# Kernel tuning notes

Hardware: AMD Instinct MI355X
Metric: run time of the kernel (lower is better)

The kernel has to match this reference:

```python
import jax, jax.numpy as jnp
import numpy as np

NUM_ATOMS = 1024
NUM_FEATS = 80      # c
NUM_IRREPS = 48     # (l_max+1)^2 * 3 with l_max=3
K3, K2, K1 = 1270, 24, 3  # CG-basis param counts per correlation order


def setup_inputs() -> dict:
    key = jax.random.key(0)
    ks = jax.random.split(key, 7)
    return {
        "node_feats": jax.random.normal(ks[0], (NUM_ATOMS, NUM_FEATS, NUM_IRREPS), jnp.float32),
        "U3": jax.random.normal(ks[1], (NUM_IRREPS, NUM_IRREPS, NUM_IRREPS, K3), jnp.float32),
        "U2": jax.random.normal(ks[2], (NUM_IRREPS, NUM_IRREPS, K2), jnp.float32),
        "U1": jax.random.normal(ks[3], (NUM_IRREPS, K1), jnp.float32),
        "W3": jax.random.normal(ks[4], (K3, NUM_FEATS), jnp.float32),
        "W2": jax.random.normal(ks[5], (K2, NUM_FEATS), jnp.float32),
        "W1": jax.random.normal(ks[6], (K1, NUM_FEATS), jnp.float32),
    }


def reference(node_feats, U3, U2, U1, W3, W2, W1):
    # equation_main: '...ik,kc,bci -> bc...' with U3 [p,q,i,k]
    # -> out [n, c, p, q]
    out = jnp.einsum('pqik,kc,nci->ncpq', U3, W3, node_feats)

    # corr = 2: c_tensor = einsum('...k,kc->c...', U2, W2) -> [c, p, q]
    c2 = jnp.einsum('pqk,kc->cpq', U2, W2) + out          # [n, c, p, q]
    # equation_contract: 'bc...i,bci->bc...'
    out = jnp.einsum('ncpi,nci->ncp', c2, node_feats)     # [n, c, p]

    # corr = 1: c_tensor = einsum('...k,kc->c...', U1, W1) -> [c, p]
    c1 = jnp.einsum('pk,kc->cp', U1, W1) + out            # [n, c, p]
    out = jnp.einsum('nci,nci->nc', c1, node_feats)       # [n, c]
    return out
```

## Files before the change

kernel.cpp:

```cpp
#include <hip/hip_runtime.h>
#include <hip/hip_bf16.h>

#define NA 1024
#define NC 80
#define NI 48
#define PQ (NI*NI)
#define M3 (PQ*NI)
#define K3 1270
#define K3P 1280
#define K2 24
#define K1 3

typedef __attribute__((ext_vector_type(8))) short bf16x8;
typedef __attribute__((ext_vector_type(4))) float f32x4;
typedef __attribute__((ext_vector_type(4))) unsigned int u32x4;

union BFPack { bf16x8 v; __hip_bfloat162 h[4]; };
union BF4 { uint2 u; __hip_bfloat162 h[2]; };
union BF2 { unsigned int u; __hip_bfloat162 h; };

__device__ __forceinline__ bf16x8 pack8(float a, float b, float c, float d,
                                        float e, float f, float g, float h) {
    BFPack u;
    u.h[0] = __float22bfloat162_rn(float2{a, b});
    u.h[1] = __float22bfloat162_rn(float2{c, d});
    u.h[2] = __float22bfloat162_rn(float2{e, f});
    u.h[3] = __float22bfloat162_rn(float2{g, h});
    return u.v;
}

__global__ __launch_bounds__(256) void k_prep(const float* __restrict__ W3,
                                              const float* __restrict__ U2,
                                              const float* __restrict__ W2,
                                              __hip_bfloat16* __restrict__ W3bt,
                                              float* __restrict__ c2t) {
    int b = blockIdx.x;
    if (b < NC) {
        int c = b;
        for (int k = threadIdx.x; k < K3P; k += 256) {
            float v = (k < K3) ? W3[(size_t)k * NC + c] : 0.f;
            W3bt[(size_t)c * K3P + k] = __float2bfloat16(v);
        }
    } else {
        int idx = (b - NC) * 256 + threadIdx.x;
        if (idx >= NC * PQ) return;
        int c  = idx / PQ;
        int pq = idx - c * PQ;
        float s = 0.f;
#pragma unroll
        for (int k = 0; k < K2; ++k) s += U2[pq * K2 + k] * W2[k * NC + c];
        c2t[idx] = s;
    }
}

__global__ __launch_bounds__(256) void k_uw3(const float* __restrict__ U3,
                                             const __hip_bfloat16* __restrict__ W3bt,
                                             __hip_bfloat16* __restrict__ UW3tb) {
    __shared__ __align__(16) unsigned short As[64 * 128];
    __shared__ __align__(16) unsigned short Bs[80 * 128];

    const int t    = threadIdx.x;
    const int wave = t >> 6;
    const int lane = t & 63;
    const int col  = lane & 15;
    const int quad = lane >> 4;

    const int m_base = blockIdx.x * 64;

    const float* __restrict__ aw = U3 + (size_t)(m_base + 16 * wave) * K3 + 2 * lane;
    char* asw = (char*)As + (16 * wave) * 256 + (lane & 3) * 4;
    const int ag = lane >> 2;

    f32x4 acc[5];
#pragma unroll
    for (int j = 0; j < 5; ++j) acc[j] = (f32x4)(0.f);

    float2 pA0[16], pA1[16];
    u32x4  pB[5];

    auto loadA = [&](float2* dst, int tl) {
        const float* an = aw + tl * 128;
        if (tl == 9) {
#pragma unroll
            for (int s = 0; s < 16; ++s)
                dst[s] = (lane < 59) ? *(const float2*)(an + (size_t)s * K3)
                                     : float2{0.f, 0.f};
        } else {
#pragma unroll
            for (int s = 0; s < 16; ++s)
                dst[s] = *(const float2*)(an + (size_t)s * K3);
        }
    };
    auto loadB = [&](int tl) {
        const int k0 = tl * 128;
#pragma unroll
        for (int u = 0; u < 5; ++u) {
            int G = t + 256 * u, c = G >> 4, g = G & 15;
            pB[u] = *(const u32x4*)(W3bt + (size_t)c * K3P + k0 + g * 8);
        }
    };
    auto writeA = [&](const float2* src) {
#pragma unroll
        for (int s = 0; s < 16; ++s) {
            BF2 w; w.h = __float22bfloat162_rn(src[s]);
            *(unsigned int*)(asw + s * 256 + ((ag ^ (s & 7)) * 16)) = w.u;
        }
    };
    auto writeB = [&]() {
#pragma unroll
        for (int u = 0; u < 5; ++u) {
            int G = t + 256 * u, c = G >> 4, g = G & 15;
            *(u32x4*)((char*)Bs + c * 256 + ((g ^ (c & 7)) * 16)) = pB[u];
        }
    };
    auto compute = [&]() {
        const int rbase = (16 * wave + col) * 256;
#pragma unroll
        for (int ks = 0; ks < 4; ++ks) {
            const int go = ((ks * 4 + quad) ^ (col & 7)) * 16;
            bf16x8 af = *(const bf16x8*)((const char*)As + rbase + go);
#pragma unroll
            for (int j = 0; j < 5; ++j) {
                bf16x8 bf = *(const bf16x8*)((const char*)Bs + (16 * j + col) * 256 + go);
                acc[j] = __builtin_amdgcn_mfma_f32_16x16x32_bf16(af, bf, acc[j], 0, 0, 0);
            }
        }
    };

    loadA(pA0, 0);
    loadB(0);
    loadA(pA1, 1);

#pragma unroll 1
    for (int t2 = 0; t2 < 5; ++t2) {
        const int tileA = 2 * t2;
        const int tileB = 2 * t2 + 1;

        __syncthreads();
        writeA(pA0);
        writeB();
        __syncthreads();
        if (tileA + 2 <= 9) loadA(pA0, tileA + 2);
        loadB(tileB);
        compute();

        __syncthreads();
        writeA(pA1);
        writeB();
        __syncthreads();
        if (tileB + 2 <= 9) loadA(pA1, tileB + 2);
        if (tileB + 1 <= 9) loadB(tileB + 1);
        compute();
    }

#pragma unroll
    for (int j = 0; j < 5; ++j) {
        int c = 16 * j + col;
        size_t o = (size_t)c * M3 + m_base + 16 * wave + quad * 4;
        BF4 pk;
        pk.h[0] = __float22bfloat162_rn(float2{acc[j].x, acc[j].y});
        pk.h[1] = __float22bfloat162_rn(float2{acc[j].z, acc[j].w});
        *(uint2*)&UW3tb[o] = pk.u;
    }
}

__global__ __launch_bounds__(256) void k_main(const float* __restrict__ nf,
                                              const __hip_bfloat16* __restrict__ UW3tb,
                                              const float* __restrict__ c2t,
                                              const float* __restrict__ U1,
                                              const float* __restrict__ W1,
                                              float* __restrict__ out) {
    __shared__ __align__(16) float Vs[64 * 52];
    __shared__ __align__(16) union { unsigned short vb[64 * 64];
                                     float red[64 * 17]; } VbRed;
    __shared__ __align__(16) unsigned short Ts[64 * 64];
    __shared__ __align__(16) float c2s[64];
    __shared__ __align__(16) float c1s[NI];

    const int t    = threadIdx.x;
    const int wave = t >> 6;
    const int col  = t & 15;
    const int quad = (t >> 4) & 3;

    const int bid = blockIdx.x;
    const int xcd = bid & 7;
    const int kb_ = bid >> 3;
    const int c   = xcd + 8 * (kb_ >> 4);
    const int nb  = kb_ & 15;
    const int n0  = nb * 64;

#pragma unroll
    for (int u = 0; u < 3; ++u) {
        int f   = t + 256 * u;
        int row = f / 12;
        int seg = f - row * 12;
        float4 v = *(const float4*)&nf[((size_t)(n0 + row) * NC + c) * NI + seg * 4];
        *(float4*)&Vs[row * 52 + seg * 4] = v;
        BF4 pk;
        pk.h[0] = __float22bfloat162_rn(float2{v.x, v.y});
        pk.h[1] = __float22bfloat162_rn(float2{v.z, v.w});
        *(uint2*)((char*)VbRed.vb + row * 128 + ((seg * 8) ^ ((row & 7) << 4))) = pk.u;
    }
    if (t < 128) {
        int row = t >> 1;
        int off = ((6 + (t & 1)) * 16) ^ ((row & 7) << 4);
        u32x4 z = (u32x4)(0u);
        *(u32x4*)((char*)VbRed.vb + row * 128 + off) = z;
        *(u32x4*)((char*)Ts       + row * 128 + off) = z;
    }
    if (t < NI) {
        float s = 0.f;
#pragma unroll
        for (int k = 0; k < K1; ++k) s += U1[t * K1 + k] * W1[k * NC + c];
        c1s[t] = s;
    }

    const __hip_bfloat16* Tcb = UW3tb + (size_t)c * M3;
    u32x4 pre0, pre1;
    pre0 = *(const u32x4*)(Tcb + (size_t)t * 8);
    if (t < 128) pre1 = *(const u32x4*)(Tcb + (size_t)(t + 256) * 8);

    __syncthreads();

    bf16x8 bfr[2][4];
#pragma unroll
    for (int s = 0; s < 2; ++s)
#pragma unroll
        for (int g = 0; g < 4; ++g) {
            int rw = 16 * g + col;
            bfr[s][g] = *(const bf16x8*)((const char*)VbRed.vb + rw * 128 +
                                         ((s * 64 + quad * 16) ^ ((rw & 7) << 4)));
        }
    int n52[4];
#pragma unroll
    for (int g = 0; g < 4; ++g) n52[g] = (16 * g + col) * 52;

    const int arow  = 16 * wave + col;
    const int abase = arow * 128;
    const int aswz  = (arow & 7) << 4;
    const int wq16  = 16 * wave + quad * 4;

    float oacc[4] = {0.f, 0.f, 0.f, 0.f};

    for (int tile = 0; tile < PQ / 64; ++tile) {
        __syncthreads();
        {
            int row = t / 6, seg = t - row * 6;
            *(u32x4*)((char*)Ts + row * 128 + ((seg * 16) ^ ((row & 7) << 4))) = pre0;
            if (t < 128) {
                int f2 = t + 256;
                int row2 = f2 / 6, seg2 = f2 - row2 * 6;
                *(u32x4*)((char*)Ts + row2 * 128 + ((seg2 * 16) ^ ((row2 & 7) << 4))) = pre1;
            }
        }
        if (t < 64) c2s[t] = c2t[(size_t)c * PQ + tile * 64 + t];
        __syncthreads();

        {
            int nt = (tile + 1 < PQ / 64) ? tile + 1 : tile;
            const __hip_bfloat16* src = Tcb + (size_t)nt * (64 * NI);
            pre0 = *(const u32x4*)(src + (size_t)t * 8);
            if (t < 128) pre1 = *(const u32x4*)(src + (size_t)(t + 256) * 8);
        }

        f32x4 acc[4];
#pragma unroll
        for (int g = 0; g < 4; ++g) acc[g] = (f32x4)(0.f);
#pragma unroll
        for (int s = 0; s < 2; ++s) {
            bf16x8 af = *(const bf16x8*)((const char*)Ts + abase +
                                         ((s * 64 + quad * 16) ^ aswz));
#pragma unroll
            for (int g = 0; g < 4; ++g)
                acc[g] = __builtin_amdgcn_mfma_f32_16x16x32_bf16(af, bfr[s][g], acc[g], 0, 0, 0);
        }

        int pqb = tile * 64 + wq16;
        int p   = (pqb * 21846) >> 20;
        int q0  = pqb - p * 48;
        f32x4 cv = *(const f32x4*)&c2s[wq16];
#pragma unroll
        for (int g = 0; g < 4; ++g) {
            float vp = Vs[n52[g] + p];
            f32x4 vq = *(const f32x4*)&Vs[n52[g] + q0];
#pragma unroll
            for (int r = 0; r < 4; ++r)
                oacc[g] += (acc[g][r] + cv[r]) * vp * vq[r];
        }
    }

    __syncthreads();
#pragma unroll
    for (int g = 0; g < 4; ++g)
        VbRed.red[(16 * g + col) * 17 + (t >> 4)] = oacc[g];
    __syncthreads();
    if (t < 64) {
        float s = 0.f;
#pragma unroll
        for (int j = 0; j < 16; ++j) s += VbRed.red[t * 17 + j];
#pragma unroll
        for (int p = 0; p < NI; ++p) s += c1s[p] * Vs[t * 52 + p];
        out[(size_t)(n0 + t) * NC + c] = s;
    }
}

extern "C" void kernel_launch(void* const* d_in, const int* in_sizes, int n_in,
                              void* d_out, int out_size, void* d_ws, size_t ws_size,
                              hipStream_t stream) {
    const float* nf = (const float*)d_in[0];
    const float* U3 = (const float*)d_in[1];
    const float* U2 = (const float*)d_in[2];
    const float* U1 = (const float*)d_in[3];
    const float* W3 = (const float*)d_in[4];
    const float* W2 = (const float*)d_in[5];
    const float* W1 = (const float*)d_in[6];
    float* out = (float*)d_out;

    __hip_bfloat16* UW3tb = (__hip_bfloat16*)d_ws;
    float* c2tw = (float*)((char*)d_ws + (size_t)NC * M3 * 2);
    __hip_bfloat16* W3bt = (__hip_bfloat16*)((char*)d_ws +
                           (size_t)NC * M3 * 2 + (size_t)NC * PQ * 4);

    k_prep<<<NC + (NC * PQ + 255) / 256, 256, 0, stream>>>(W3, U2, W2, W3bt, c2tw);
    k_uw3 <<<M3 / 64,                    256, 0, stream>>>(U3, W3bt, UW3tb);
    k_main<<<NC * 16,                    256, 0, stream>>>(nf, UW3tb, c2tw, U1, W1, out);
}
```

Measured before the change: 817.8 us.

## Pre-convert U3 to padded bf16 in a separate kernel before the GEMM

Adds a k_cvt kernel that converts U3 (110592x1270 fp32, about 562MB) into a padded bf16 buffer with a 1280 stride. The UW3 GEMM then reads that buffer with 16-byte vector loads and a single-stage register prefetch, replacing the strided float2 loads that converted in registers and double-buffered. The goal is cheaper, more coalesced A-tile loads and less register pressure, but the fp32 U3 must still be read once and an extra ~283MB bf16 copy written and read again. That extra traffic may cost more than the load path saves.

After: 936.6 us. +14.5%, slower.

```diff
diff --git a/kernel.cpp b/kernel.cpp
--- a/kernel.cpp
+++ b/kernel.cpp
@@ -19,14 +19,17 @@
 union BF4 { uint2 u; __hip_bfloat162 h[2]; };
 union BF2 { unsigned int u; __hip_bfloat162 h; };
 
-__device__ __forceinline__ bf16x8 pack8(float a, float b, float c, float d,
-                                        float e, float f, float g, float h) {
-    BFPack u;
-    u.h[0] = __float22bfloat162_rn(float2{a, b});
-    u.h[1] = __float22bfloat162_rn(float2{c, d});
-    u.h[2] = __float22bfloat162_rn(float2{e, f});
-    u.h[3] = __float22bfloat162_rn(float2{g, h});
-    return u.v;
+__global__ __launch_bounds__(256) void k_cvt(const float* __restrict__ U3,
+                                             __hip_bfloat16* __restrict__ U3b) {
+    for (int m = blockIdx.x; m < M3; m += gridDim.x) {
+        const float2* __restrict__ src = (const float2*)(U3 + (size_t)m * K3);
+        unsigned int* __restrict__ dst = (unsigned int*)(U3b + (size_t)m * K3P);
+        for (int j = threadIdx.x; j < 635; j += 256) {
+            BF2 w; w.h = __float22bfloat162_rn(src[j]);
+            dst[j] = w.u;
+        }
+        if (threadIdx.x < 5) dst[635 + threadIdx.x] = 0u;
+    }
 }
 
 __global__ __launch_bounds__(256) void k_prep(const float* __restrict__ W3,
@@ -53,7 +56,7 @@
     }
 }
 
-__global__ __launch_bounds__(256) void k_uw3(const float* __restrict__ U3,
+__global__ __launch_bounds__(256) void k_uw3(const __hip_bfloat16* __restrict__ U3b,
                                              const __hip_bfloat16* __restrict__ W3bt,
                                              __hip_bfloat16* __restrict__ UW3tb) {
     __shared__ __align__(16) unsigned short As[64 * 128];
@@ -67,29 +70,21 @@
 
     const int m_base = blockIdx.x * 64;
 
-    const float* __restrict__ aw = U3 + (size_t)(m_base + 16 * wave) * K3 + 2 * lane;
-    char* asw = (char*)As + (16 * wave) * 256 + (lane & 3) * 4;
-    const int ag = lane >> 2;
+    const char* __restrict__ aw = (const char*)U3b +
+        (size_t)(m_base + 16 * wave + (lane >> 4)) * (K3P * 2) + (lane & 15) * 16;
 
     f32x4 acc[5];
 #pragma unroll
     for (int j = 0; j < 5; ++j) acc[j] = (f32x4)(0.f);
 
-    float2 pA0[16], pA1[16];
-    u32x4  pB[5];
-
-    auto loadA = [&](float2* dst, int tl) {
-        const float* an = aw + tl * 128;
-        if (tl == 9) {
-#pragma unroll
-            for (int s = 0; s < 16; ++s)
-                dst[s] = (lane < 59) ? *(const float2*)(an + (size_t)s * K3)
-                                     : float2{0.f, 0.f};
-        } else {
-#pragma unroll
-            for (int s = 0; s < 16; ++s)
-                dst[s] = *(const float2*)(an + (size_t)s * K3);
-        }
+    u32x4 pA[4];
+    u32x4 pB[5];
+
+    auto loadA = [&](int tl) {
+        const char* src = aw + tl * 256;
+#pragma unroll
+        for (int i = 0; i < 4; ++i)
+            pA[i] = *(const u32x4*)(src + (size_t)i * 4 * (K3P * 2));
     };
     auto loadB = [&](int tl) {
         const int k0 = tl * 128;
@@ -99,11 +94,11 @@
             pB[u] = *(const u32x4*)(W3bt + (size_t)c * K3P + k0 + g * 8);
         }
     };
-    auto writeA = [&](const float2* src) {
-#pragma unroll
-        for (int s = 0; s < 16; ++s) {
-            BF2 w; w.h = __float22bfloat162_rn(src[s]);
-            *(unsigned int*)(asw + s * 256 + ((ag ^ (s & 7)) * 16)) = w.u;
+    auto writeA = [&]() {
+#pragma unroll
+        for (int i = 0; i < 4; ++i) {
+            int r = 16 * wave + 4 * i + (lane >> 4);
+            *(u32x4*)((char*)As + r * 256 + (((lane & 15) ^ (r & 7)) * 16)) = pA[i];
         }
     };
     auto writeB = [&]() {
@@ -127,29 +122,16 @@
         }
     };
 
-    loadA(pA0, 0);
+    loadA(0);
     loadB(0);
-    loadA(pA1, 1);
 
 #pragma unroll 1
-    for (int t2 = 0; t2 < 5; ++t2) {
-        const int tileA = 2 * t2;
-        const int tileB = 2 * t2 + 1;
-
+    for (int tile = 0; tile < 10; ++tile) {
         __syncthreads();
-        writeA(pA0);
+        writeA();
         writeB();
         __syncthreads();
-        if (tileA + 2 <= 9) loadA(pA0, tileA + 2);
-        loadB(tileB);
-        compute();
-
-        __syncthreads();
-        writeA(pA1);
-        writeB();
-        __syncthreads();
-        if (tileB + 2 <= 9) loadA(pA1, tileB + 2);
-        if (tileB + 1 <= 9) loadB(tileB + 1);
+        if (tile < 9) { loadA(tile + 1); loadB(tile + 1); }
         compute();
     }
 
@@ -316,12 +298,17 @@
     const float* W1 = (const float*)d_in[6];
     float* out = (float*)d_out;
 
-    __hip_bfloat16* UW3tb = (__hip_bfloat16*)d_ws;
-    float* c2tw = (float*)((char*)d_ws + (size_t)NC * M3 * 2);
-    __hip_bfloat16* W3bt = (__hip_bfloat16*)((char*)d_ws +
-                           (size_t)NC * M3 * 2 + (size_t)NC * PQ * 4);
-
+    char* ws = (char*)d_ws;
+    __hip_bfloat16* UW3tb = (__hip_bfloat16*)ws;
+    ws += (size_t)NC * M3 * 2;
+    float* c2tw = (float*)ws;
+    ws += (size_t)NC * PQ * 4;
+    __hip_bfloat16* W3bt = (__hip_bfloat16*)ws;
+    ws += (size_t)NC * K3P * 2;
+    __hip_bfloat16* U3b = (__hip_bfloat16*)ws;
+
+    k_cvt <<<3456,                       256, 0, stream>>>(U3, U3b);
     k_prep<<<NC + (NC * PQ + 255) / 256, 256, 0, stream>>>(W3, U2, W2, W3bt, c2tw);
-    k_uw3 <<<M3 / 64,                    256, 0, stream>>>(U3, W3bt, UW3tb);
+    k_uw3 <<<M3 / 64,                    256, 0, stream>>>(U3b, W3bt, UW3tb);
     k_main<<<NC * 16,                    256, 0, stream>>>(nf, UW3tb, c2tw, U1, W1, out);
 }
```
